# Optimization experiments

Measured on AMD Instinct MI355X. Metric: run time of the kernel, lower is better.

## Reference

```python
import jax, jax.numpy as jnp
import numpy as np

N, Q, E, D = 100000, 128, 500000, 32
D4 = 4 * D
RATIO_UPDATE = 0.2
NEG_SLOPE = 0.01  # LeakyReLU default


def setup_inputs() -> dict:
    key = jax.random.key(0)
    ks = jax.random.split(key, 16)
    return {
        "visited_node_score": jax.random.uniform(ks[0], (N,), jnp.float32),
        "node_repr": jax.random.normal(ks[1], (N, D), jnp.float32),
        "eg0": jnp.sort(jax.random.randint(ks[2], (E,), 0, Q)),
        "src0": jax.random.randint(ks[3], (E,), 0, N),
        "dst0": jax.random.randint(ks[4], (E,), 0, N),
        "rel0": jax.random.normal(ks[5], (E, D), jnp.float32),
        "eg1": jnp.sort(jax.random.randint(ks[6], (E,), 0, Q)),
        "src1": jax.random.randint(ks[7], (E,), 0, N),
        "dst1": jax.random.randint(ks[8], (E,), 0, N),
        "rel1": jax.random.normal(ks[9], (E, D), jnp.float32),
        "query_src_emb": jax.random.normal(ks[10], (Q, D), jnp.float32),
        "query_rel_emb": jax.random.normal(ks[11], (Q, D), jnp.float32),
        "Wq": jax.random.normal(ks[12], (D4, D4), jnp.float32) * np.sqrt(2.0 / D4).astype(np.float32),
        "Wk": jax.random.normal(ks[13], (D4, D4), jnp.float32) * np.sqrt(2.0 / D4).astype(np.float32),
        "Wlin": jax.random.normal(ks[14], (D, D), jnp.float32) * np.sqrt(2.0 / (2 * D)).astype(np.float32),
        "blin": jnp.zeros((D,), jnp.float32),
        "max_edges": 500,
    }


def segment_softmax(logits, seg, num_segments):
    # softmax within groups of identical seg id (source node index)
    m = jax.ops.segment_max(logits, seg, num_segments=num_segments)
    ex = jnp.exp(logits - m[seg])
    s = jax.ops.segment_sum(ex, seg, num_segments=num_segments)
    return ex / s[seg]


def segment_topk_mask(values, seg, k):
    # keep mask for per-segment top-k (seg must be sorted); stable -> first occurrence on ties
    n = values.shape[0]
    order = jnp.lexsort((-values, seg))  # primary: seg, secondary: descending value
    seg_sorted = seg[order]
    idx = jnp.arange(n)
    is_start = jnp.concatenate([jnp.array([True]), seg_sorted[1:] != seg_sorted[:-1]])
    seg_start = jax.lax.cummax(jnp.where(is_start, idx, 0))
    rank_sorted = idx - seg_start  # rank within segment, 0 = largest
    rank = jnp.zeros((n,), jnp.int32).at[order].set(rank_sorted.astype(jnp.int32))
    return rank < k


def reference(visited_node_score, node_repr, eg0, src0, dst0, rel0,
              eg1, src1, dst1, rel1, query_src_emb, query_rel_emb,
              Wq, Wk, Wlin, blin, max_edges):
    def att_logits(repr_, src, dst, eg, rel):
        q = query_src_emb[eg]
        r = query_rel_emb[eg]
        left = jnp.concatenate([repr_[src], rel, q, r], axis=-1)   # [E, 4D]
        right = jnp.concatenate([repr_[dst], rel, q, r], axis=-1)  # [E, 4D]
        return jnp.sum((left @ Wq.T) * (right @ Wk.T), axis=-1)    # [E]

    num_nodes = node_repr.shape[0]

    # ---- last layer: attention + segmented top-k pruning ----
    logits1 = att_logits(node_repr, src1, dst1, eg1, rel1)
    w1 = segment_softmax(logits1, src1, num_nodes)           # softmax over out-edges of each src node
    src_score = visited_node_score[src1]
    target_score = w1 * src_score
    keep = segment_topk_mask(target_score, eg1, max_edges)   # top-k per eg_idx
    w1p = jnp.where(keep, w1, 0.0)

    # node score aggregation == 'sum': score[n] = sum_{kept e: dst=n} w * src_score
    updated_node_score = jax.ops.segment_sum(w1p * src_score, dst1, num_segments=num_nodes)

    # representation update along pruned edges (linear_act=False)
    agg = jax.ops.segment_sum(w1p[:, None] * node_repr[src1], dst1, num_segments=num_nodes)
    repr_ = (1.0 - RATIO_UPDATE) * agg + RATIO_UPDATE * node_repr

    # ---- earlier layer(s), no pruning ----
    logits0 = att_logits(repr_, src0, dst0, eg0, rel0)
    w0 = segment_softmax(logits0, src0, num_nodes)
    agg0 = jax.ops.segment_sum(w0[:, None] * repr_[src0], dst0, num_segments=num_nodes)
    repr_ = (1.0 - RATIO_UPDATE) * agg0 + RATIO_UPDATE * repr_

    # bypass_forward: LeakyReLU(Linear(repr))
    h = repr_ @ Wlin.T + blin
    updated_repr = jnp.where(h >= 0, h, NEG_SLOPE * h)
    return updated_node_score, updated_repr
```

## Files before the change

### kernel.cpp

```cpp
#include <hip/hip_runtime.h>
#include <math.h>

#define DD 32
#define DD4 128
#define TPB 256
#define LDSCAP 6144
#define CANDCAP 2048

__device__ __forceinline__ unsigned long long dsort_key(double x) {
  unsigned long long b = (unsigned long long)__double_as_longlong(x);
  return (b & 0x8000000000000000ull) ? ~b : (b | 0x8000000000000000ull);
}
__device__ __forceinline__ double dunsort_key(unsigned long long k) {
  unsigned long long b = (k & 0x8000000000000000ull) ? (k ^ 0x8000000000000000ull) : ~k;
  return __longlong_as_double((long long)b);
}
__device__ __forceinline__ unsigned int fsort_key(float x) {
  unsigned int b = __float_as_uint(x);
  return (b & 0x80000000u) ? ~b : (b | 0x80000000u);
}
__device__ __forceinline__ float funsort_key(unsigned int k) {
  unsigned int b = (k & 0x80000000u) ? (k ^ 0x80000000u) : ~k;
  return __uint_as_float(b);
}

__device__ __forceinline__ int block_iscan256(int x, int* wsum) {
  const int lane = threadIdx.x & 63, w = threadIdx.x >> 6;
#pragma unroll
  for (int o = 1; o < 64; o <<= 1) {
    int y = __shfl_up(x, o, 64);
    if (lane >= o) x += y;
  }
  if (lane == 63) wsum[w] = x;
  __syncthreads();
  int add = 0;
#pragma unroll
  for (int i = 0; i < 4; ++i) add += (i < w) ? wsum[i] : 0;
  __syncthreads();
  return x + add;
}

__global__ __launch_bounds__(TPB) void k_precompute_M(
    const float* __restrict__ Wq, const float* __restrict__ Wk,
    double* __restrict__ M64, float* __restrict__ M32) {
  int t = blockIdx.x * blockDim.x + threadIdx.x;
  int i = t >> 7, j = t & 127;
  double acc = 0.0;
  for (int k = 0; k < DD4; ++k)
    acc += (double)Wq[k * DD4 + i] * (double)Wk[k * DD4 + j];
  M64[i * DD4 + j] = acc;
  M32[i * DD4 + j] = (float)acc;
}

__global__ __launch_bounds__(TPB) void k_sym22(
    const double* __restrict__ M64, double* __restrict__ S64, float* __restrict__ S32) {
  int i = blockIdx.x * blockDim.x + threadIdx.x;
  int r = i >> 5, c = i & 31;
  double g  = M64[(32 + r) * DD4 + 32 + c];
  double gt = M64[(32 + c) * DD4 + 32 + r];
  double s = (c > r) ? (g + gt) : ((c == r) ? g : 0.0);
  S64[i] = s;
  S32[i] = (float)s;
}

__global__ __launch_bounds__(64) void k_per_query(
    const double* __restrict__ M64,
    const float* __restrict__ qemb, const float* __restrict__ remb,
    double* __restrict__ p64, double* __restrict__ pD64, double* __restrict__ c64,
    float* __restrict__ p32, float* __restrict__ pD32, float* __restrict__ c32) {
  int q = blockIdx.x;
  int l = threadIdx.x;
  __shared__ double qr[64];
  qr[l] = (l < DD) ? (double)qemb[q * DD + l] : (double)remb[q * DD + (l - DD)];
  __syncthreads();
  double a = 0.0;
  for (int j = 0; j < 64; ++j) a += M64[l * DD4 + 64 + j] * qr[j];
  double ct = 0.0;
  for (int j = 0; j < 64; ++j) ct += M64[(64 + j) * DD4 + l] * qr[j];
  if (l >= DD) a += ct;
  p64[q * 64 + l] = a;
  p32[q * 64 + l] = (float)a;
  if (l < DD) {
    pD64[q * DD + l] = ct;
    pD32[q * DD + l] = (float)ct;
  }
  double a3 = 0.0;
  for (int j = 0; j < 64; ++j) a3 += M64[(64 + l) * DD4 + 64 + j] * qr[j];
  a3 *= qr[l];
  for (int o = 32; o; o >>= 1) a3 += __shfl_xor(a3, o);
  if (l == 0) { c64[q] = a3; c32[q] = (float)a3; }
}

#define G_T(c) Mmat[(c) * DD4 + j]
#define G_U(c) Mmat[j * DD4 + 32 + (c)]
#define G_V(c) Mmat[(32 + (c)) * DD4 + j]

#define NP_TILE(GEXPR)                                                          \
  for (int tt = 0; tt < 4; ++tt) {                                              \
    T a0=(T)0,a1=(T)0,a2=(T)0,a3=(T)0,a4=(T)0,a5=(T)0,a6=(T)0,a7=(T)0;          \
    const int c0 = tt * 8;                                                      \
    _Pragma("unroll")                                                           \
    for (int j = 0; j < 32; ++j) {                                              \
      const T hj = hh[j];                                                       \
      a0 += (GEXPR(c0 + 0)) * hj; a1 += (GEXPR(c0 + 1)) * hj;                   \
      a2 += (GEXPR(c0 + 2)) * hj; a3 += (GEXPR(c0 + 3)) * hj;                   \
      a4 += (GEXPR(c0 + 4)) * hj; a5 += (GEXPR(c0 + 5)) * hj;                   \
      a6 += (GEXPR(c0 + 6)) * hj; a7 += (GEXPR(c0 + 7)) * hj;                   \
    }                                                                           \
    xq[tid * 9 + tt * 2]     = make_float4((float)a0,(float)a1,(float)a2,(float)a3); \
    xq[tid * 9 + tt * 2 + 1] = make_float4((float)a4,(float)a5,(float)a6,(float)a7); \
  }

#define NP_STORE(dst)                                                           \
  __syncthreads();                                                              \
  {                                                                             \
    float4* go = (float4*)(dst) + (size_t)nbase * 8;                            \
    _Pragma("unroll")                                                           \
    for (int k = 0; k < 8; ++k) {                                               \
      int f = k * TPB + tid;                                                    \
      if ((f >> 3) < nlim) go[f] = xq[(f >> 3) * 9 + (f & 7)];                  \
    }                                                                           \
  }                                                                             \
  __syncthreads();

template <typename T, bool MIX>
__global__ __launch_bounds__(TPB) void k_node_pre(
    const T* __restrict__ Mmat, const float* __restrict__ reprIn,
    const float* __restrict__ aggIn, float* __restrict__ reprOut,
    float* __restrict__ t, float* __restrict__ u, float* __restrict__ v, int N_) {
  __shared__ float xp[TPB * 36];
  float4* xq = (float4*)xp;
  const int tid = threadIdx.x;
  const int nbase = blockIdx.x * TPB;
  const int n = nbase + tid;
  const int nlim = min(TPB, N_ - nbase);
  const bool valid = tid < nlim;
  T hh[32];
  if (valid) {
    const float4* h4 = (const float4*)reprIn + (size_t)n * 8;
#pragma unroll
    for (int jq = 0; jq < 8; ++jq) {
      float4 x = h4[jq];
      if constexpr (MIX) {
        const float4 a = ((const float4*)aggIn)[(size_t)n * 8 + jq];
        x = make_float4(0.8f * a.x + 0.2f * x.x, 0.8f * a.y + 0.2f * x.y,
                        0.8f * a.z + 0.2f * x.z, 0.8f * a.w + 0.2f * x.w);
        xq[tid * 9 + jq] = x;
      }
      hh[4 * jq]     = (T)x.x; hh[4 * jq + 1] = (T)x.y;
      hh[4 * jq + 2] = (T)x.z; hh[4 * jq + 3] = (T)x.w;
    }
  } else {
#pragma unroll
    for (int j = 0; j < 32; ++j) hh[j] = (T)0;
  }
  if constexpr (MIX) {
    NP_STORE(reprOut)
  }
  NP_TILE(G_T)
  NP_STORE(t)
  NP_TILE(G_U)
  NP_STORE(u)
  NP_TILE(G_V)
  NP_STORE(v)
}

template <typename T>
__global__ __launch_bounds__(TPB) void k_quad(
    const T* __restrict__ Smat,
    const float* __restrict__ rel, const int* __restrict__ eg,
    const T* __restrict__ pq, const T* __restrict__ cq,
    T* __restrict__ quad, int E) {
  const int e = blockIdx.x * TPB + threadIdx.x;
  if (e >= E) return;
  const int q = eg[e];
  T rl[32];
  {
    const float4* r4 = (const float4*)rel + (size_t)e * 8;
#pragma unroll
    for (int j = 0; j < 8; ++j) {
      float4 x = r4[j];
      rl[4 * j] = (T)x.x; rl[4 * j + 1] = (T)x.y;
      rl[4 * j + 2] = (T)x.z; rl[4 * j + 3] = (T)x.w;
    }
  }
  const T* prow = pq + (size_t)q * 64 + 32;
  T lin0 = (T)0, lin1 = (T)0;
#pragma unroll
  for (int i = 0; i < 32; i += 2) {
    lin0 += prow[i] * rl[i];
    lin1 += prow[i + 1] * rl[i + 1];
  }
  T a0 = cq[q] + lin0, a1 = lin1, a2 = (T)0, a3 = (T)0;
#pragma unroll
  for (int i = 0; i < 32; ++i) {
    T r0 = Smat[i * 32 + i] * rl[i];
    T r1 = (T)0;
#pragma unroll
    for (int j = i + 1; j < 32; ++j) {
      if ((j - i) & 1) r1 += Smat[i * 32 + j] * rl[j];
      else             r0 += Smat[i * 32 + j] * rl[j];
    }
    T rr = (r0 + r1) * rl[i];
    if ((i & 3) == 0) a0 += rr;
    else if ((i & 3) == 1) a1 += rr;
    else if ((i & 3) == 2) a2 += rr;
    else a3 += rr;
  }
  quad[e] = (a0 + a1) + (a2 + a3);
}

template <typename T>
__global__ __launch_bounds__(TPB) void k_edge_dots(
    const float* __restrict__ repr, const float* __restrict__ rel,
    const int* __restrict__ src, const int* __restrict__ dst, const int* __restrict__ eg,
    const float* __restrict__ tvec, const float* __restrict__ uvec, const float* __restrict__ vvec,
    const T* __restrict__ pq, const T* __restrict__ pDq, const T* __restrict__ quad,
    T* __restrict__ logits, void* __restrict__ mkey, int E) {
  const long long t = (long long)blockIdx.x * TPB + threadIdx.x;
  const int part = (int)(t & 7);
  const int e0 = (int)((t >> 3) * 2);
  if (e0 >= E) return;
  const int e1 = e0 + 1;
  const bool has1 = (e1 < E);
  const int s0 = src[e0], d0 = dst[e0], q0 = eg[e0];
  const int s1 = has1 ? src[e1] : s0;
  const int d1 = has1 ? dst[e1] : d0;
  const int q1 = has1 ? eg[e1] : q0;
  const float4* R  = (const float4*)repr;
  const float4* Tv = (const float4*)tvec;
  const float4* Uv = (const float4*)uvec;
  const float4* Vv = (const float4*)vvec;
  const float4* RL = (const float4*)rel;
  const float4 hs0 = R[(size_t)s0 * 8 + part],  hs1 = R[(size_t)s1 * 8 + part];
  const float4 td0 = Tv[(size_t)d0 * 8 + part], td1 = Tv[(size_t)d1 * 8 + part];
  const float4 hd0 = R[(size_t)d0 * 8 + part],  hd1 = R[(size_t)d1 * 8 + part];
  const float4 us0 = Uv[(size_t)s0 * 8 + part], us1 = Uv[(size_t)s1 * 8 + part];
  const float4 vd0 = Vv[(size_t)d0 * 8 + part], vd1 = Vv[(size_t)d1 * 8 + part];
  const float4 rl0 = RL[(size_t)e0 * 8 + part];
  const float4 rl1 = has1 ? RL[(size_t)e1 * 8 + part] : rl0;
  const T* p0  = pq  + (size_t)q0 * 64 + part * 4;
  const T* p1  = pq  + (size_t)q1 * 64 + part * 4;
  const T* pD0 = pDq + (size_t)q0 * DD + part * 4;
  const T* pD1 = pDq + (size_t)q1 * DD + part * 4;
  T a = (T)hs0.x * ((T)td0.x + p0[0]) + (T)hs0.y * ((T)td0.y + p0[1]) +
        (T)hs0.z * ((T)td0.z + p0[2]) + (T)hs0.w * ((T)td0.w + p0[3]);
  a += (T)hd0.x * pD0[0] + (T)hd0.y * pD0[1] + (T)hd0.z * pD0[2] + (T)hd0.w * pD0[3];
  a += (T)rl0.x * (T)(us0.x + vd0.x) + (T)rl0.y * (T)(us0.y + vd0.y) +
       (T)rl0.z * (T)(us0.z + vd0.z) + (T)rl0.w * (T)(us0.w + vd0.w);
  T b = (T)hs1.x * ((T)td1.x + p1[0]) + (T)hs1.y * ((T)td1.y + p1[1]) +
        (T)hs1.z * ((T)td1.z + p1[2]) + (T)hs1.w * ((T)td1.w + p1[3]);
  b += (T)hd1.x * pD1[0] + (T)hd1.y * pD1[1] + (T)hd1.z * pD1[2] + (T)hd1.w * pD1[3];
  b += (T)rl1.x * (T)(us1.x + vd1.x) + (T)rl1.y * (T)(us1.y + vd1.y) +
       (T)rl1.z * (T)(us1.z + vd1.z) + (T)rl1.w * (T)(us1.w + vd1.w);
  a += __shfl_xor(a, 1); a += __shfl_xor(a, 2); a += __shfl_xor(a, 4);
  b += __shfl_xor(b, 1); b += __shfl_xor(b, 2); b += __shfl_xor(b, 4);
  if (part == 0) {
    a += quad[e0];
    logits[e0] = a;
    if constexpr (sizeof(T) == 8) {
      atomicMax((unsigned long long*)mkey + s0, dsort_key((double)a));
    } else {
      atomicMax((unsigned int*)mkey + s0, fsort_key((float)a));
    }
    if (has1) {
      b += quad[e1];
      logits[e1] = b;
      if constexpr (sizeof(T) == 8) {
        atomicMax((unsigned long long*)mkey + s1, dsort_key((double)b));
      } else {
        atomicMax((unsigned int*)mkey + s1, fsort_key((float)b));
      }
    }
  }
}

__global__ __launch_bounds__(TPB) void k_expsum64(
    double* __restrict__ io, const unsigned long long* __restrict__ mkey,
    const int* __restrict__ src, double* __restrict__ ssum, int E) {
  int e = blockIdx.x * blockDim.x + threadIdx.x;
  if (e >= E) return;
  int s = src[e];
  double ex = exp(io[e] - dunsort_key(mkey[s]));
  io[e] = ex;
  atomicAdd(&ssum[s], ex);
}
__global__ __launch_bounds__(TPB) void k_expsum32h(
    float* __restrict__ io, const unsigned int* __restrict__ mkey,
    const int* __restrict__ src, const int* __restrict__ dst,
    float* __restrict__ ssum, int* __restrict__ cnt, int E) {
  int e = blockIdx.x * blockDim.x + threadIdx.x;
  if (e >= E) return;
  int s = src[e];
  float ex = expf(io[e] - funsort_key(mkey[s]));
  io[e] = ex;
  atomicAdd(&ssum[s], ex);
  atomicAdd(&cnt[dst[e]], 1);
}

__global__ __launch_bounds__(TPB) void k_weights_target(
    const double* __restrict__ ex, const double* __restrict__ ssum,
    const int* __restrict__ src, const float* __restrict__ score,
    const int* __restrict__ eg, int* __restrict__ qoff,
    float* __restrict__ w1f, unsigned int* __restrict__ tkey, int E, int Q) {
  int e = blockIdx.x * blockDim.x + threadIdx.x;
  if (e >= E) return;
  int s = src[e];
  double w = ex[e] / ssum[s];
  float wf = (float)w;
  w1f[e] = wf;
  float tgt = wf * score[s];
  tkey[e] = fsort_key(tgt);
  int cur = eg[e];
  int prev = (e == 0) ? -1 : eg[e - 1];
  for (int v = prev + 1; v <= cur; ++v) qoff[v] = e;
  if (e == E - 1) {
    for (int v = cur + 1; v <= Q; ++v) qoff[v] = E;
  }
}

__global__ __launch_bounds__(TPB) void k_topk(
    const unsigned int* __restrict__ tkey, const float* __restrict__ w1f,
    const int* __restrict__ qoff, const int* __restrict__ maxe,
    float* __restrict__ w1p, int E) {
  __shared__ unsigned int keys[LDSCAP];
  __shared__ int hist[256];
  __shared__ unsigned short cand[CANDCAP];
  __shared__ int wsum[4];
  __shared__ int sh_cnt;
  __shared__ unsigned int sh_prefix;
  __shared__ int sh_need;
  const int q = blockIdx.x;
  const int s = qoff[q], e2 = qoff[q + 1];
  const int n = e2 - s;
  const int K = maxe[0];
  if (n <= K) {
    for (int i = s + threadIdx.x; i < e2; i += TPB) w1p[i] = w1f[i];
    return;
  }
  const bool useLds = (n <= LDSCAP);
  if (useLds) {
    for (int i = threadIdx.x; i < n; i += TPB) keys[i] = tkey[s + i];
  }
  hist[threadIdx.x] = 0;
  __syncthreads();
  for (int i = threadIdx.x; i < n; i += TPB) {
    unsigned int k = useLds ? keys[i] : tkey[s + i];
    atomicAdd(&hist[k >> 24], 1);
  }
  __syncthreads();
  int need = K;
  {
    int h = hist[255 - threadIdx.x];
    int incl = block_iscan256(h, wsum);
    int excl = incl - h;
    if (incl >= need && excl < need) {
      sh_prefix = (unsigned int)(255 - threadIdx.x) << 24;
      sh_need = need - excl;
    }
  }
  __syncthreads();
  unsigned int prefix = sh_prefix;
  need = sh_need;
  const int cnt0 = hist[prefix >> 24];
  const bool compact = useLds && (cnt0 <= CANDCAP);
  if (threadIdx.x == 0) sh_cnt = 0;
  __syncthreads();
  if (compact) {
    const unsigned int d0 = prefix >> 24;
    for (int i = threadIdx.x; i < n; i += TPB) {
      if ((keys[i] >> 24) == d0) {
        int p = atomicAdd(&sh_cnt, 1);
        cand[p] = (unsigned short)i;
      }
    }
  }
  __syncthreads();
  const int ncand = compact ? sh_cnt : 0;
  for (int pass = 1; pass < 4; ++pass) {
    const int shift = 24 - 8 * pass;
    const unsigned int himask = 0xFFFFFFFFu << (shift + 8);
    hist[threadIdx.x] = 0;
    __syncthreads();
    if (compact) {
      for (int ci = threadIdx.x; ci < ncand; ci += TPB) {
        unsigned int k = keys[cand[ci]];
        if ((k & himask) == prefix) atomicAdd(&hist[(k >> shift) & 255], 1);
      }
    } else {
      for (int i = threadIdx.x; i < n; i += TPB) {
        unsigned int k = useLds ? keys[i] : tkey[s + i];
        if ((k & himask) == prefix) atomicAdd(&hist[(k >> shift) & 255], 1);
      }
    }
    __syncthreads();
    int h = hist[255 - threadIdx.x];
    int incl = block_iscan256(h, wsum);
    int excl = incl - h;
    if (incl >= need && excl < need) {
      sh_prefix = prefix | ((unsigned int)(255 - threadIdx.x) << shift);
      sh_need = need - excl;
    }
    __syncthreads();
    prefix = sh_prefix;
    need = sh_need;
    __syncthreads();
  }
  const unsigned int kth = prefix;
  const int r = need;
  const int C = (n + TPB - 1) / TPB;
  const int b0 = min(threadIdx.x * C, n);
  const int b1 = min(b0 + C, n);
  int myt = 0;
  for (int i = b0; i < b1; ++i) {
    unsigned int k = useLds ? keys[i] : tkey[s + i];
    myt += (k == kth) ? 1 : 0;
  }
  int tincl = block_iscan256(myt, wsum);
  int tiepre = tincl - myt;
  for (int i = b0; i < b1; ++i) {
    unsigned int k = useLds ? keys[i] : tkey[s + i];
    float v = 0.f;
    if (k > kth) {
      v = w1f[s + i];
    } else if (k == kth) {
      if (tiepre < r) v = w1f[s + i];
      ++tiepre;
    }
    w1p[s + i] = v;
  }
}

__global__ __launch_bounds__(TPB) void k_apply1(
    const float* __restrict__ w1p, const int* __restrict__ src, const int* __restrict__ dst,
    const float* __restrict__ repr0, const float* __restrict__ score,
    float* __restrict__ agg, float* __restrict__ score_out, int E) {
  int t = blockIdx.x * blockDim.x + threadIdx.x;
  int e = t >> 3, part = t & 7;
  if (e >= E) return;
  float w = w1p[e];
  if (w == 0.f) return;
  int sv = src[e], dv = dst[e];
  const float4 rv = ((const float4*)repr0)[sv * 8 + part];
  float* ap = agg + (size_t)dv * DD + part * 4;
  atomicAdd(ap + 0, w * rv.x);
  atomicAdd(ap + 1, w * rv.y);
  atomicAdd(ap + 2, w * rv.z);
  atomicAdd(ap + 3, w * rv.w);
  if (part == 0) atomicAdd(score_out + dv, w * score[sv]);
}

#define SCHUNK 1024
__global__ __launch_bounds__(TPB) void k_scan1(
    const int* __restrict__ cnt, int* __restrict__ off, int* __restrict__ bsum, int N_) {
  __shared__ int sd[TPB];
  const int b = blockIdx.x, t = threadIdx.x;
  const int base = b * SCHUNK + t * 4;
  int v[4];
  int s4 = 0;
#pragma unroll
  for (int k = 0; k < 4; ++k) {
    v[k] = (base + k < N_) ? cnt[base + k] : 0;
    s4 += v[k];
  }
  sd[t] = s4;
  __syncthreads();
  for (int o = 1; o < TPB; o <<= 1) {
    int x = (t >= o) ? sd[t - o] : 0;
    __syncthreads();
    sd[t] += x;
    __syncthreads();
  }
  int excl = sd[t] - s4;
  if (t == TPB - 1) bsum[b] = sd[t];
  int run = excl;
#pragma unroll
  for (int k = 0; k < 4; ++k) {
    if (base + k < N_) { off[base + k] = run; run += v[k]; }
  }
}

__global__ __launch_bounds__(TPB) void k_scan2(
    int* __restrict__ bsum, int* __restrict__ off, int nblk, int N_, int E) {
  __shared__ int wsum[4];
  if (nblk <= TPB) {
    int t = threadIdx.x;
    int x = (t < nblk) ? bsum[t] : 0;
    int orig = x;
    const int lane = t & 63, w = t >> 6;
#pragma unroll
    for (int o = 1; o < 64; o <<= 1) {
      int y = __shfl_up(x, o, 64);
      if (lane >= o) x += y;
    }
    if (lane == 63) wsum[w] = x;
    __syncthreads();
    int add = 0;
#pragma unroll
    for (int i = 0; i < 4; ++i) add += (i < w) ? wsum[i] : 0;
    x += add;
    if (t < nblk) bsum[t] = x - orig;
    if (t == 0) off[N_] = E;
  } else {
    if (threadIdx.x != 0) return;
    int run = 0;
    for (int i = 0; i < nblk; ++i) { int tmp = bsum[i]; bsum[i] = run; run += tmp; }
    off[N_] = E;
  }
}

__global__ __launch_bounds__(TPB) void k_scan3(
    int* __restrict__ off, const int* __restrict__ bsum, int* __restrict__ cursor, int N_) {
  int i = blockIdx.x * blockDim.x + threadIdx.x;
  if (i >= N_) return;
  int v = off[i] + bsum[i >> 10];
  off[i] = v;
  cursor[i] = v;
}

__global__ __launch_bounds__(TPB) void k_scatter0(
    const float* __restrict__ ex, const float* __restrict__ ssum,
    const int* __restrict__ src, const int* __restrict__ dst,
    int* __restrict__ cursor, float2* __restrict__ pk, int E) {
  int e = blockIdx.x * blockDim.x + threadIdx.x;
  if (e >= E) return;
  int s = src[e];
  float w = ex[e] / ssum[s];
  int pos = atomicAdd(&cursor[dst[e]], 1);
  pk[pos] = make_float2(w, __int_as_float(s));
}

__global__ __launch_bounds__(TPB) void k_gather_mix(
    const float2* __restrict__ pk, const int* __restrict__ off,
    const float* __restrict__ repr1, float* __restrict__ mixbuf, int N_) {
  const int n = blockIdx.x * 8 + (threadIdx.x >> 5);
  const int c = threadIdx.x & 31;
  if (n >= N_) return;
  const float self = repr1[(size_t)n * DD + c];
  float acc = 0.f;
  const int j0 = off[n], j1 = off[n + 1];
  int j = j0;
  for (; j + 4 <= j1; j += 4) {
    const float2 p0 = pk[j], p1 = pk[j + 1], p2 = pk[j + 2], p3 = pk[j + 3];
    const float g0 = repr1[(size_t)__float_as_int(p0.y) * DD + c];
    const float g1 = repr1[(size_t)__float_as_int(p1.y) * DD + c];
    const float g2 = repr1[(size_t)__float_as_int(p2.y) * DD + c];
    const float g3 = repr1[(size_t)__float_as_int(p3.y) * DD + c];
    acc += p0.x * g0;
    acc += p1.x * g1;
    acc += p2.x * g2;
    acc += p3.x * g3;
  }
  for (; j < j1; ++j) {
    const float2 p = pk[j];
    acc += p.x * repr1[(size_t)__float_as_int(p.y) * DD + c];
  }
  mixbuf[(size_t)n * DD + c] = 0.8f * acc + 0.2f * self;
}

__global__ __launch_bounds__(TPB) void k_final_linear(
    const float* __restrict__ Wlin, const float* __restrict__ blin,
    const float* __restrict__ mixbuf, float* __restrict__ out_repr, int N_) {
  __shared__ float xp[TPB * 36];
  float4* xq = (float4*)xp;
  const int tid = threadIdx.x;
  const int nbase = blockIdx.x * TPB;
  const int n = nbase + tid;
  const int nlim = min(TPB, N_ - nbase);
  float m[32];
  if (tid < nlim) {
    const float4* h4 = (const float4*)mixbuf + (size_t)n * 8;
#pragma unroll
    for (int jq = 0; jq < 8; ++jq) {
      float4 x = h4[jq];
      m[4 * jq] = x.x; m[4 * jq + 1] = x.y; m[4 * jq + 2] = x.z; m[4 * jq + 3] = x.w;
    }
  } else {
#pragma unroll
    for (int j = 0; j < 32; ++j) m[j] = 0.f;
  }
  for (int tt = 0; tt < 4; ++tt) {
    const int c0 = tt * 8;
    float a0 = blin[c0 + 0], a1 = blin[c0 + 1], a2 = blin[c0 + 2], a3 = blin[c0 + 3];
    float a4 = blin[c0 + 4], a5 = blin[c0 + 5], a6 = blin[c0 + 6], a7 = blin[c0 + 7];
#pragma unroll
    for (int j = 0; j < 32; ++j) {
      const float hj = m[j];
      a0 += Wlin[(c0 + 0) * DD + j] * hj; a1 += Wlin[(c0 + 1) * DD + j] * hj;
      a2 += Wlin[(c0 + 2) * DD + j] * hj; a3 += Wlin[(c0 + 3) * DD + j] * hj;
      a4 += Wlin[(c0 + 4) * DD + j] * hj; a5 += Wlin[(c0 + 5) * DD + j] * hj;
      a6 += Wlin[(c0 + 6) * DD + j] * hj; a7 += Wlin[(c0 + 7) * DD + j] * hj;
    }
    a0 = (a0 >= 0.f) ? a0 : 0.01f * a0; a1 = (a1 >= 0.f) ? a1 : 0.01f * a1;
    a2 = (a2 >= 0.f) ? a2 : 0.01f * a2; a3 = (a3 >= 0.f) ? a3 : 0.01f * a3;
    a4 = (a4 >= 0.f) ? a4 : 0.01f * a4; a5 = (a5 >= 0.f) ? a5 : 0.01f * a5;
    a6 = (a6 >= 0.f) ? a6 : 0.01f * a6; a7 = (a7 >= 0.f) ? a7 : 0.01f * a7;
    xq[tid * 9 + tt * 2]     = make_float4(a0, a1, a2, a3);
    xq[tid * 9 + tt * 2 + 1] = make_float4(a4, a5, a6, a7);
  }
  NP_STORE(out_repr)
}

extern "C" void kernel_launch(void* const* d_in, const int* in_sizes, int n_in,
                              void* d_out, int out_size, void* d_ws, size_t ws_size,
                              hipStream_t stream) {
  (void)n_in; (void)out_size; (void)ws_size;
  const float* score = (const float*)d_in[0];
  const float* nrepr = (const float*)d_in[1];
  const int*   eg0   = (const int*)d_in[2];
  const int*   src0  = (const int*)d_in[3];
  const int*   dst0  = (const int*)d_in[4];
  const float* rel0  = (const float*)d_in[5];
  const int*   eg1   = (const int*)d_in[6];
  const int*   src1  = (const int*)d_in[7];
  const int*   dst1  = (const int*)d_in[8];
  const float* rel1  = (const float*)d_in[9];
  const float* qemb  = (const float*)d_in[10];
  const float* remb  = (const float*)d_in[11];
  const float* Wq    = (const float*)d_in[12];
  const float* Wk    = (const float*)d_in[13];
  const float* Wlin  = (const float*)d_in[14];
  const float* blin  = (const float*)d_in[15];
  const int*   maxe  = (const int*)d_in[16];

  const int N_ = in_sizes[0];
  const int E_ = in_sizes[2];
  const int Q_ = in_sizes[10] / DD;

  char* wsc = (char*)d_ws;
  size_t off = 0;
  auto alloc = [&](size_t bytes) -> void* {
    void* p = wsc + off;
    off += (bytes + 255) & ~(size_t)255;
    return p;
  };
  double* M64  = (double*)alloc((size_t)DD4 * DD4 * 8);
  float*  M32  = (float*)alloc((size_t)DD4 * DD4 * 4);
  double* S64  = (double*)alloc((size_t)DD * DD * 8);
  float*  S32  = (float*)alloc((size_t)DD * DD * 4);
  double* p64  = (double*)alloc((size_t)Q_ * 64 * 8);
  double* pD64 = (double*)alloc((size_t)Q_ * DD * 8);
  double* c64  = (double*)alloc((size_t)Q_ * 8);
  float*  p32  = (float*)alloc((size_t)Q_ * 64 * 4);
  float*  pD32 = (float*)alloc((size_t)Q_ * DD * 4);
  float*  c32  = (float*)alloc((size_t)Q_ * 4);
  int*    qoff = (int*)alloc((size_t)(Q_ + 2) * 4);
  double* lg1  = (double*)alloc((size_t)E_ * 8);
  double* qv64 = (double*)alloc((size_t)E_ * 8);
  float*  w1f  = (float*)alloc((size_t)E_ * 4);
  unsigned int* tkey = (unsigned int*)alloc((size_t)E_ * 4);
  float*  w1p  = (float*)alloc((size_t)E_ * 4);
  float*  lg0  = (float*)alloc((size_t)E_ * 4);
  float*  repr1 = (float*)alloc((size_t)N_ * DD * 4);
  float*  tvec = (float*)alloc((size_t)N_ * DD * 4);
  float*  uvec = (float*)alloc((size_t)N_ * DD * 4);
  float*  vvec = (float*)alloc((size_t)N_ * DD * 4);
  size_t zstart = off;
  unsigned long long* mkey1 = (unsigned long long*)alloc((size_t)N_ * 8);
  double* s1   = (double*)alloc((size_t)N_ * 8);
  float*  agg  = (float*)alloc((size_t)N_ * DD * 4);
  unsigned int* mkey0 = (unsigned int*)alloc((size_t)N_ * 4);
  float*  s0   = (float*)alloc((size_t)N_ * 4);
  size_t zlen = off - zstart;

  float* qv32 = (float*)qv64;

  int* cnt    = (int*)tvec;
  int* offcsr = (int*)tvec + N_;
  int* cursor = (int*)tvec + 2 * (size_t)N_ + 64;
  int* bsum   = (int*)tvec + 3 * (size_t)N_ + 128;
  float2* pk  = (float2*)uvec;
  float* mixbuf = vvec;

  float* out_score = (float*)d_out;
  float* out_repr  = out_score + N_;

  hipMemsetAsync(wsc + zstart, 0, zlen, stream);
  hipMemsetAsync(d_out, 0, (size_t)N_ * 4, stream);

  k_precompute_M<<<(DD4 * DD4) / TPB, TPB, 0, stream>>>(Wq, Wk, M64, M32);
  k_sym22<<<4, TPB, 0, stream>>>(M64, S64, S32);
  k_per_query<<<Q_, 64, 0, stream>>>(M64, qemb, remb, p64, pD64, c64, p32, pD32, c32);

  const int ngrid = (N_ + TPB - 1) / TPB;
  const int egrid = (E_ + TPB - 1) / TPB;
  const int dgrid1 = (int)(((size_t)E_ * 8 + TPB - 1) / TPB);
  const int dgrid2 = (int)(((size_t)((E_ + 1) / 2) * 8 + TPB - 1) / TPB);

  k_node_pre<double, false><<<ngrid, TPB, 0, stream>>>(M64, nrepr, nullptr, nullptr,
                                                       tvec, uvec, vvec, N_);
  k_quad<double><<<egrid, TPB, 0, stream>>>(S64, rel1, eg1, p64, c64, qv64, E_);
  k_edge_dots<double><<<dgrid2, TPB, 0, stream>>>(nrepr, rel1, src1, dst1, eg1,
                                                  tvec, uvec, vvec, p64, pD64, qv64,
                                                  lg1, (void*)mkey1, E_);
  k_expsum64<<<egrid, TPB, 0, stream>>>(lg1, mkey1, src1, s1, E_);
  k_weights_target<<<egrid, TPB, 0, stream>>>(lg1, s1, src1, score, eg1, qoff,
                                              w1f, tkey, E_, Q_);
  k_topk<<<Q_, TPB, 0, stream>>>(tkey, w1f, qoff, maxe, w1p, E_);

  k_apply1<<<dgrid1, TPB, 0, stream>>>(w1p, src1, dst1, nrepr, score, agg, out_score, E_);

  k_node_pre<float, true><<<ngrid, TPB, 0, stream>>>(M32, nrepr, agg, repr1,
                                                     tvec, uvec, vvec, N_);
  k_quad<float><<<egrid, TPB, 0, stream>>>(S32, rel0, eg0, p32, c32, qv32, E_);
  k_edge_dots<float><<<dgrid2, TPB, 0, stream>>>(repr1, rel0, src0, dst0, eg0,
                                                 tvec, uvec, vvec, p32, pD32, qv32,
                                                 lg0, (void*)mkey0, E_);

  hipMemsetAsync(cnt, 0, (size_t)N_ * 4, stream);
  k_expsum32h<<<egrid, TPB, 0, stream>>>(lg0, mkey0, src0, dst0, s0, cnt, E_);
  const int nblk = (N_ + SCHUNK - 1) / SCHUNK;
  k_scan1<<<nblk, TPB, 0, stream>>>(cnt, offcsr, bsum, N_);
  k_scan2<<<1, TPB, 0, stream>>>(bsum, offcsr, nblk, N_, E_);
  k_scan3<<<ngrid, TPB, 0, stream>>>(offcsr, bsum, cursor, N_);
  k_scatter0<<<egrid, TPB, 0, stream>>>(lg0, s0, src0, dst0, cursor, pk, E_);
  k_gather_mix<<<(N_ + 7) / 8, TPB, 0, stream>>>(pk, offcsr, repr1, mixbuf, N_);
  k_final_linear<<<ngrid, TPB, 0, stream>>>(Wlin, blin, mixbuf, out_repr, N_);
}
```

Before: 623.4 us.

## Fuse weight/target computation into top-k and simplify edge-dot kernel

Removes the separate weights/target kernel. The query-offset computation moves into the exp-sum kernel, and the softmax-weight and target-key computation moves into the per-query top-k kernel, which keeps the values in LDS or writes them to global only for oversized segments. It also reverts edge_dots to one edge per 8-thread group and uses nontemporal loads for the streamed relation embeddings. The aim is to cut one launch and the write/read round trip of w1f/tkey, at the cost of doing the division serially inside only 128 top-k blocks and adding LDS use there.

```diff
diff --git a/kernel.cpp b/kernel.cpp
--- a/kernel.cpp
+++ b/kernel.cpp
@@ -22,6 +22,12 @@
 __device__ __forceinline__ float funsort_key(unsigned int k) {
   unsigned int b = (k & 0x80000000u) ? (k ^ 0x80000000u) : ~k;
   return __uint_as_float(b);
+}
+
+typedef float f32x4 __attribute__((ext_vector_type(4)));
+__device__ __forceinline__ float4 nt_load4(const float* p) {
+  f32x4 v = __builtin_nontemporal_load((const f32x4*)p);
+  return make_float4(v.x, v.y, v.z, v.w);
 }
 
 __device__ __forceinline__ int block_iscan256(int x, int* wsum) {
@@ -176,10 +182,10 @@
   const int q = eg[e];
   T rl[32];
   {
-    const float4* r4 = (const float4*)rel + (size_t)e * 8;
+    const float* rbase = rel + (size_t)e * 32;
 #pragma unroll
     for (int j = 0; j < 8; ++j) {
-      float4 x = r4[j];
+      float4 x = nt_load4(rbase + j * 4);
       rl[4 * j] = (T)x.x; rl[4 * j + 1] = (T)x.y;
       rl[4 * j + 2] = (T)x.z; rl[4 * j + 3] = (T)x.w;
     }
@@ -218,72 +224,52 @@
     const T* __restrict__ pq, const T* __restrict__ pDq, const T* __restrict__ quad,
     T* __restrict__ logits, void* __restrict__ mkey, int E) {
   const long long t = (long long)blockIdx.x * TPB + threadIdx.x;
-  const int part = (int)(t & 7);
-  const int e0 = (int)((t >> 3) * 2);
-  if (e0 >= E) return;
-  const int e1 = e0 + 1;
-  const bool has1 = (e1 < E);
-  const int s0 = src[e0], d0 = dst[e0], q0 = eg[e0];
-  const int s1 = has1 ? src[e1] : s0;
-  const int d1 = has1 ? dst[e1] : d0;
-  const int q1 = has1 ? eg[e1] : q0;
-  const float4* R  = (const float4*)repr;
-  const float4* Tv = (const float4*)tvec;
-  const float4* Uv = (const float4*)uvec;
-  const float4* Vv = (const float4*)vvec;
-  const float4* RL = (const float4*)rel;
-  const float4 hs0 = R[(size_t)s0 * 8 + part],  hs1 = R[(size_t)s1 * 8 + part];
-  const float4 td0 = Tv[(size_t)d0 * 8 + part], td1 = Tv[(size_t)d1 * 8 + part];
-  const float4 hd0 = R[(size_t)d0 * 8 + part],  hd1 = R[(size_t)d1 * 8 + part];
-  const float4 us0 = Uv[(size_t)s0 * 8 + part], us1 = Uv[(size_t)s1 * 8 + part];
-  const float4 vd0 = Vv[(size_t)d0 * 8 + part], vd1 = Vv[(size_t)d1 * 8 + part];
-  const float4 rl0 = RL[(size_t)e0 * 8 + part];
-  const float4 rl1 = has1 ? RL[(size_t)e1 * 8 + part] : rl0;
-  const T* p0  = pq  + (size_t)q0 * 64 + part * 4;
-  const T* p1  = pq  + (size_t)q1 * 64 + part * 4;
-  const T* pD0 = pDq + (size_t)q0 * DD + part * 4;
-  const T* pD1 = pDq + (size_t)q1 * DD + part * 4;
-  T a = (T)hs0.x * ((T)td0.x + p0[0]) + (T)hs0.y * ((T)td0.y + p0[1]) +
-        (T)hs0.z * ((T)td0.z + p0[2]) + (T)hs0.w * ((T)td0.w + p0[3]);
-  a += (T)hd0.x * pD0[0] + (T)hd0.y * pD0[1] + (T)hd0.z * pD0[2] + (T)hd0.w * pD0[3];
-  a += (T)rl0.x * (T)(us0.x + vd0.x) + (T)rl0.y * (T)(us0.y + vd0.y) +
-       (T)rl0.z * (T)(us0.z + vd0.z) + (T)rl0.w * (T)(us0.w + vd0.w);
-  T b = (T)hs1.x * ((T)td1.x + p1[0]) + (T)hs1.y * ((T)td1.y + p1[1]) +
-        (T)hs1.z * ((T)td1.z + p1[2]) + (T)hs1.w * ((T)td1.w + p1[3]);
-  b += (T)hd1.x * pD1[0] + (T)hd1.y * pD1[1] + (T)hd1.z * pD1[2] + (T)hd1.w * pD1[3];
-  b += (T)rl1.x * (T)(us1.x + vd1.x) + (T)rl1.y * (T)(us1.y + vd1.y) +
-       (T)rl1.z * (T)(us1.z + vd1.z) + (T)rl1.w * (T)(us1.w + vd1.w);
-  a += __shfl_xor(a, 1); a += __shfl_xor(a, 2); a += __shfl_xor(a, 4);
-  b += __shfl_xor(b, 1); b += __shfl_xor(b, 2); b += __shfl_xor(b, 4);
+  const int e = (int)(t >> 3), part = (int)(t & 7);
+  if (e >= E) return;
+  const int s = src[e], d = dst[e], q = eg[e];
+  const float4 hs = ((const float4*)repr)[(size_t)s * 8 + part];
+  const float4 td = ((const float4*)tvec)[(size_t)d * 8 + part];
+  const float4 hd = ((const float4*)repr)[(size_t)d * 8 + part];
+  const float4 rl = nt_load4(rel + ((size_t)e * 8 + part) * 4);
+  const float4 us = ((const float4*)uvec)[(size_t)s * 8 + part];
+  const float4 vd = ((const float4*)vvec)[(size_t)d * 8 + part];
+  const T* p  = pq  + (size_t)q * 64 + part * 4;
+  const T* pD = pDq + (size_t)q * DD + part * 4;
+  T a = (T)hs.x * ((T)td.x + p[0]) + (T)hs.y * ((T)td.y + p[1]) +
+        (T)hs.z * ((T)td.z + p[2]) + (T)hs.w * ((T)td.w + p[3]);
+  a += (T)hd.x * pD[0] + (T)hd.y * pD[1] + (T)hd.z * pD[2] + (T)hd.w * pD[3];
+  a += (T)rl.x * (T)(us.x + vd.x) + (T)rl.y * (T)(us.y + vd.y) +
+       (T)rl.z * (T)(us.z + vd.z) + (T)rl.w * (T)(us.w + vd.w);
+  a += __shfl_xor(a, 1);
+  a += __shfl_xor(a, 2);
+  a += __shfl_xor(a, 4);
   if (part == 0) {
-    a += quad[e0];
-    logits[e0] = a;
+    a += quad[e];
+    logits[e] = a;
     if constexpr (sizeof(T) == 8) {
-      atomicMax((unsigned long long*)mkey + s0, dsort_key((double)a));
+      atomicMax((unsigned long long*)mkey + s, dsort_key((double)a));
     } else {
-      atomicMax((unsigned int*)mkey + s0, fsort_key((float)a));
-    }
-    if (has1) {
-      b += quad[e1];
-      logits[e1] = b;
-      if constexpr (sizeof(T) == 8) {
-        atomicMax((unsigned long long*)mkey + s1, dsort_key((double)b));
-      } else {
-        atomicMax((unsigned int*)mkey + s1, fsort_key((float)b));
-      }
+      atomicMax((unsigned int*)mkey + s, fsort_key((float)a));
     }
   }
 }
 
 __global__ __launch_bounds__(TPB) void k_expsum64(
     double* __restrict__ io, const unsigned long long* __restrict__ mkey,
-    const int* __restrict__ src, double* __restrict__ ssum, int E) {
+    const int* __restrict__ src, const int* __restrict__ eg,
+    double* __restrict__ ssum, int* __restrict__ qoff, int E, int Q) {
   int e = blockIdx.x * blockDim.x + threadIdx.x;
   if (e >= E) return;
   int s = src[e];
   double ex = exp(io[e] - dunsort_key(mkey[s]));
   io[e] = ex;
   atomicAdd(&ssum[s], ex);
+  int cur = eg[e];
+  int prev = (e == 0) ? -1 : eg[e - 1];
+  for (int v = prev + 1; v <= cur; ++v) qoff[v] = e;
+  if (e == E - 1) {
+    for (int v = cur + 1; v <= Q; ++v) qoff[v] = E;
+  }
 }
 __global__ __launch_bounds__(TPB) void k_expsum32h(
     float* __restrict__ io, const unsigned int* __restrict__ mkey,
@@ -298,32 +284,14 @@
   atomicAdd(&cnt[dst[e]], 1);
 }
 
-__global__ __launch_bounds__(TPB) void k_weights_target(
+__global__ __launch_bounds__(TPB) void k_topk(
     const double* __restrict__ ex, const double* __restrict__ ssum,
     const int* __restrict__ src, const float* __restrict__ score,
-    const int* __restrict__ eg, int* __restrict__ qoff,
-    float* __restrict__ w1f, unsigned int* __restrict__ tkey, int E, int Q) {
-  int e = blockIdx.x * blockDim.x + threadIdx.x;
-  if (e >= E) return;
-  int s = src[e];
-  double w = ex[e] / ssum[s];
-  float wf = (float)w;
-  w1f[e] = wf;
-  float tgt = wf * score[s];
-  tkey[e] = fsort_key(tgt);
-  int cur = eg[e];
-  int prev = (e == 0) ? -1 : eg[e - 1];
-  for (int v = prev + 1; v <= cur; ++v) qoff[v] = e;
-  if (e == E - 1) {
-    for (int v = cur + 1; v <= Q; ++v) qoff[v] = E;
-  }
-}
-
-__global__ __launch_bounds__(TPB) void k_topk(
-    const unsigned int* __restrict__ tkey, const float* __restrict__ w1f,
     const int* __restrict__ qoff, const int* __restrict__ maxe,
+    unsigned int* __restrict__ tkeyg, float* __restrict__ w1fg,
     float* __restrict__ w1p, int E) {
   __shared__ unsigned int keys[LDSCAP];
+  __shared__ float wval[LDSCAP];
   __shared__ int hist[256];
   __shared__ unsigned short cand[CANDCAP];
   __shared__ int wsum[4];
@@ -335,17 +303,32 @@
   const int n = e2 - s;
   const int K = maxe[0];
   if (n <= K) {
-    for (int i = s + threadIdx.x; i < e2; i += TPB) w1p[i] = w1f[i];
+    for (int i = s + threadIdx.x; i < e2; i += TPB) {
+      int sv = src[i];
+      w1p[i] = (float)(ex[i] / ssum[sv]);
+    }
     return;
   }
   const bool useLds = (n <= LDSCAP);
   if (useLds) {
-    for (int i = threadIdx.x; i < n; i += TPB) keys[i] = tkey[s + i];
+    for (int i = threadIdx.x; i < n; i += TPB) {
+      int sv = src[s + i];
+      float wf = (float)(ex[s + i] / ssum[sv]);
+      wval[i] = wf;
+      keys[i] = fsort_key(wf * score[sv]);
+    }
+  } else {
+    for (int i = s + threadIdx.x; i < e2; i += TPB) {
+      int sv = src[i];
+      float wf = (float)(ex[i] / ssum[sv]);
+      w1fg[i] = wf;
+      tkeyg[i] = fsort_key(wf * score[sv]);
+    }
   }
   hist[threadIdx.x] = 0;
   __syncthreads();
   for (int i = threadIdx.x; i < n; i += TPB) {
-    unsigned int k = useLds ? keys[i] : tkey[s + i];
+    unsigned int k = useLds ? keys[i] : tkeyg[s + i];
     atomicAdd(&hist[k >> 24], 1);
   }
   __syncthreads();
@@ -389,7 +372,7 @@
       }
     } else {
       for (int i = threadIdx.x; i < n; i += TPB) {
-        unsigned int k = useLds ? keys[i] : tkey[s + i];
+        unsigned int k = useLds ? keys[i] : tkeyg[s + i];
         if ((k & himask) == prefix) atomicAdd(&hist[(k >> shift) & 255], 1);
       }
     }
@@ -413,18 +396,18 @@
   const int b1 = min(b0 + C, n);
   int myt = 0;
   for (int i = b0; i < b1; ++i) {
-    unsigned int k = useLds ? keys[i] : tkey[s + i];
+    unsigned int k = useLds ? keys[i] : tkeyg[s + i];
     myt += (k == kth) ? 1 : 0;
   }
   int tincl = block_iscan256(myt, wsum);
   int tiepre = tincl - myt;
   for (int i = b0; i < b1; ++i) {
-    unsigned int k = useLds ? keys[i] : tkey[s + i];
+    unsigned int k = useLds ? keys[i] : tkeyg[s + i];
     float v = 0.f;
     if (k > kth) {
-      v = w1f[s + i];
+      v = useLds ? wval[i] : w1fg[s + i];
     } else if (k == kth) {
-      if (tiepre < r) v = w1f[s + i];
+      if (tiepre < r) v = useLds ? wval[i] : w1fg[s + i];
       ++tiepre;
     }
     w1p[s + i] = v;
@@ -684,28 +667,25 @@
 
   const int ngrid = (N_ + TPB - 1) / TPB;
   const int egrid = (E_ + TPB - 1) / TPB;
-  const int dgrid1 = (int)(((size_t)E_ * 8 + TPB - 1) / TPB);
-  const int dgrid2 = (int)(((size_t)((E_ + 1) / 2) * 8 + TPB - 1) / TPB);
+  const int dgrid = (int)(((size_t)E_ * 8 + TPB - 1) / TPB);
 
   k_node_pre<double, false><<<ngrid, TPB, 0, stream>>>(M64, nrepr, nullptr, nullptr,
                                                        tvec, uvec, vvec, N_);
   k_quad<double><<<egrid, TPB, 0, stream>>>(S64, rel1, eg1, p64, c64, qv64, E_);
-  k_edge_dots<double><<<dgrid2, TPB, 0, stream>>>(nrepr, rel1, src1, dst1, eg1,
-                                                  tvec, uvec, vvec, p64, pD64, qv64,
-                                                  lg1, (void*)mkey1, E_);
-  k_expsum64<<<egrid, TPB, 0, stream>>>(lg1, mkey1, src1, s1, E_);
-  k_weights_target<<<egrid, TPB, 0, stream>>>(lg1, s1, src1, score, eg1, qoff,
-                                              w1f, tkey, E_, Q_);
-  k_topk<<<Q_, TPB, 0, stream>>>(tkey, w1f, qoff, maxe, w1p, E_);
-
-  k_apply1<<<dgrid1, TPB, 0, stream>>>(w1p, src1, dst1, nrepr, score, agg, out_score, E_);
+  k_edge_dots<double><<<dgrid, TPB, 0, stream>>>(nrepr, rel1, src1, dst1, eg1,
+                                                 tvec, uvec, vvec, p64, pD64, qv64,
+                                                 lg1, (void*)mkey1, E_);
+  k_expsum64<<<egrid, TPB, 0, stream>>>(lg1, mkey1, src1, eg1, s1, qoff, E_, Q_);
+  k_topk<<<Q_, TPB, 0, stream>>>(lg1, s1, src1, score, qoff, maxe, tkey, w1f, w1p, E_);
+
+  k_apply1<<<dgrid, TPB, 0, stream>>>(w1p, src1, dst1, nrepr, score, agg, out_score, E_);
 
   k_node_pre<float, true><<<ngrid, TPB, 0, stream>>>(M32, nrepr, agg, repr1,
                                                      tvec, uvec, vvec, N_);
   k_quad<float><<<egrid, TPB, 0, stream>>>(S32, rel0, eg0, p32, c32, qv32, E_);
-  k_edge_dots<float><<<dgrid2, TPB, 0, stream>>>(repr1, rel0, src0, dst0, eg0,
-                                                 tvec, uvec, vvec, p32, pD32, qv32,
-                                                 lg0, (void*)mkey0, E_);
+  k_edge_dots<float><<<dgrid, TPB, 0, stream>>>(repr1, rel0, src0, dst0, eg0,
+                                                tvec, uvec, vvec, p32, pD32, qv32,
+                                                lg0, (void*)mkey0, E_);
 
   hipMemsetAsync(cnt, 0, (size_t)N_ * 4, stream);
   k_expsum32h<<<egrid, TPB, 0, stream>>>(lg0, mkey0, src0, dst0, s0, cnt, E_);
```

New measurement: 640.5 us. 1.03x slower.
